# Optimization experiments

Measured on AMD Instinct MI355X. Metric: run time of the kernel, lower is better.

The kernel has to match this reference:

```python
import jax, jax.numpy as jnp
import numpy as np

N = 50000
E = 300000
HOPS = 3
LAYERS = 2
HEADS = 8
D_IN = 256
D_HID = 256
D_OUT = 256
D_HEAD = D_HID // HEADS
DECAY = [float(np.exp(-0.5 * k)) for k in range(HOPS)]  # hop_decay alpha = 0.5
LRELU_ACT = 0.01   # nn.LeakyReLU default slope (activation)
LRELU_ATT = 0.2    # GATConv attention leaky_relu slope
LN_EPS = 1e-5


def setup_inputs() -> dict:
    key = jax.random.key(0)
    ks = jax.random.split(key, 12)
    def sc(fan):
        return 1.0 / np.sqrt(fan)
    inp = {
        "x": jax.random.normal(ks[0], (N, D_IN), jnp.float32),
        "edge_index_k_hops": jax.random.randint(ks[1], (HOPS, 2, E), 0, N, jnp.int32),
        "lin1_w": jax.random.normal(ks[2], (D_IN, D_HID), jnp.float32) * sc(D_IN),
        "lin1_b": jnp.zeros((D_HID,), jnp.float32),
        "gat_w": jax.random.normal(ks[3], (LAYERS, HOPS, D_HID, D_HID), jnp.float32) * sc(D_HID),
        "gat_att_src": jax.random.normal(ks[4], (LAYERS, HOPS, HEADS, D_HEAD), jnp.float32) * sc(D_HEAD),
        "gat_att_dst": jax.random.normal(ks[5], (LAYERS, HOPS, HEADS, D_HEAD), jnp.float32) * sc(D_HEAD),
        "gat_bias": jnp.zeros((LAYERS, HOPS, D_HID), jnp.float32),
        "dec_w": jax.random.normal(ks[6], (LAYERS, HOPS, D_HID, D_OUT), jnp.float32) * sc(D_HID),
        "dec_b": jnp.zeros((LAYERS, HOPS, D_OUT), jnp.float32),
        "ln_scale": jnp.ones((LAYERS, D_OUT), jnp.float32),
        "ln_bias": jnp.zeros((LAYERS, D_OUT), jnp.float32),
    }
    return inp


def gat_conv(x, src, dst, W, a_src, a_dst, bias):
    # x: [N, D_HID]; src/dst: [E] ints. PyG GATConv (concat=True), eval mode.
    h = (x @ W).reshape(N, HEADS, D_HEAD)                  # [N, H, Dh]
    alpha_s = jnp.einsum('nhd,hd->nh', h, a_src)           # [N, H]
    alpha_d = jnp.einsum('nhd,hd->nh', h, a_dst)           # [N, H]
    e = jax.nn.leaky_relu(alpha_s[src] + alpha_d[dst], LRELU_ATT)  # [E, H]
    m = jax.ops.segment_max(e, dst, num_segments=N)        # segment softmax over dst
    e = jnp.exp(e - m[dst])
    s = jax.ops.segment_sum(e, dst, num_segments=N)
    a = e / (s[dst] + 1e-16)                               # [E, H]
    msg = h[src] * a[:, :, None]                           # [E, H, Dh]
    out = jax.ops.segment_sum(msg, dst, num_segments=N)    # [N, H, Dh]
    return out.reshape(N, D_HID) + bias


def layer_norm(x, scale, bias):
    mu = jnp.mean(x, axis=-1, keepdims=True)
    var = jnp.mean(jnp.square(x - mu), axis=-1, keepdims=True)
    return (x - mu) * jax.lax.rsqrt(var + LN_EPS) * scale + bias


def reference(x, edge_index_k_hops, lin1_w, lin1_b, gat_w, gat_att_src, gat_att_dst,
              gat_bias, dec_w, dec_b, ln_scale, ln_bias):
    h = jax.nn.leaky_relu(x @ lin1_w + lin1_b, LRELU_ACT)
    residual = h
    for l in range(LAYERS):
        acc = jnp.zeros((N, D_OUT), h.dtype)
        for k in range(HOPS):
            src = edge_index_k_hops[k, 0]
            dst = edge_index_k_hops[k, 1]
            xk = gat_conv(h, src, dst, gat_w[l, k], gat_att_src[l, k],
                          gat_att_dst[l, k], gat_bias[l, k])
            xk = jax.nn.leaky_relu(xk @ dec_w[l, k] + dec_b[l, k], LRELU_ACT)
            acc = acc + DECAY[k] * xk
        h = layer_norm(acc, ln_scale[l], ln_bias[l]) + residual
        residual = h
    return h
```

## Files before the change

kernel.cpp:

```cpp
#include <hip/hip_runtime.h>
#include <hip/hip_bf16.h>

#define NNODE 50000
#define NEDGE 300000
#define KPAD 40

static const float DECAY0 = 1.0f;
static const float DECAY1 = 0.60653065971263342f;
static const float DECAY2 = 0.36787944117144233f;

typedef __attribute__((ext_vector_type(8))) short bf16x8;
typedef __attribute__((ext_vector_type(4))) float f32x4;

__device__ __forceinline__ void split_bf16(float f, unsigned short& hi, unsigned short& lo) {
    const unsigned u = __float_as_uint(f);
    hi = (unsigned short)(u >> 16);
    const float fh = __uint_as_float((unsigned)hi << 16);
    lo = (unsigned short)(__float_as_uint(f - fh) >> 16);
}

__global__ __launch_bounds__(256) void transpose_w(
    const float* __restrict__ gat_w, const float* __restrict__ dec_w,
    const float* __restrict__ lin1_w, float* __restrict__ Wt)
{
    const int m = blockIdx.z;
    const float* src = (m < 6) ? gat_w + (size_t)m * 65536
                     : (m < 12) ? dec_w + (size_t)(m - 6) * 65536
                                : lin1_w;
    float* dst = Wt + (size_t)m * 65536;
    __shared__ float tile[32][33];
    const int bx = blockIdx.x * 32;
    const int by = blockIdx.y * 32;
    const int tx = threadIdx.x & 31;
    const int ty = threadIdx.x >> 5;
#pragma unroll
    for (int i = 0; i < 32; i += 8)
        tile[ty + i][tx] = src[(size_t)(by + ty + i) * 256 + bx + tx];
    __syncthreads();
#pragma unroll
    for (int i = 0; i < 32; i += 8)
        dst[(size_t)(bx + ty + i) * 256 + by + tx] = tile[tx][ty + i];
}

__global__ __launch_bounds__(256) void gemm_mfma(
    const float* __restrict__ A, const float* __restrict__ Wt, float* __restrict__ C,
    int M, const float* __restrict__ in_bias, const float* __restrict__ out_bias,
    float slope, int do_act, int accum, float decay)
{
    __shared__ unsigned short Ah[128][KPAD];
    __shared__ unsigned short Al[128][KPAD];
    __shared__ unsigned short Bh[128][KPAD];
    __shared__ unsigned short Bl[128][KPAD];

    const int tid  = threadIdx.x;
    const int bm   = blockIdx.x * 128;
    const int bn   = blockIdx.y * 128;
    const int lane = tid & 63;
    const int w    = tid >> 6;
    const int wm   = w >> 1, wn = w & 1;
    const int srow = tid >> 1;
    const int sks  = (tid & 1) << 4;

    f32x4 acc[4][4];
#pragma unroll
    for (int mi = 0; mi < 4; mi++)
#pragma unroll
        for (int ni = 0; ni < 4; ni++) {
            acc[mi][ni][0] = 0.f; acc[mi][ni][1] = 0.f;
            acc[mi][ni][2] = 0.f; acc[mi][ni][3] = 0.f;
        }

    const int lrow = lane & 15;
    const int koff = (lane >> 4) << 3;

    for (int k0 = 0; k0 < 256; k0 += 32) {
        __syncthreads();
        {
            float v[16];
            const int gr = bm + srow;
            if (gr < M) {
                const float* ap = A + (size_t)gr * 256 + k0 + sks;
                const float4 f0 = ((const float4*)ap)[0];
                const float4 f1 = ((const float4*)ap)[1];
                const float4 f2 = ((const float4*)ap)[2];
                const float4 f3 = ((const float4*)ap)[3];
                v[0]=f0.x; v[1]=f0.y; v[2]=f0.z; v[3]=f0.w;
                v[4]=f1.x; v[5]=f1.y; v[6]=f1.z; v[7]=f1.w;
                v[8]=f2.x; v[9]=f2.y; v[10]=f2.z; v[11]=f2.w;
                v[12]=f3.x; v[13]=f3.y; v[14]=f3.z; v[15]=f3.w;
            } else {
#pragma unroll
                for (int j = 0; j < 16; j++) v[j] = 0.f;
            }
            if (in_bias) {
#pragma unroll
                for (int j = 0; j < 16; j++) v[j] += in_bias[k0 + sks + j];
            }
            bf16x8 h0, h1, l0, l1;
#pragma unroll
            for (int j = 0; j < 8; j++) {
                unsigned short h, l;
                split_bf16(v[j], h, l);
                h0[j] = (short)h; l0[j] = (short)l;
            }
#pragma unroll
            for (int j = 0; j < 8; j++) {
                unsigned short h, l;
                split_bf16(v[8 + j], h, l);
                h1[j] = (short)h; l1[j] = (short)l;
            }
            *(bf16x8*)&Ah[srow][sks]     = h0;
            *(bf16x8*)&Ah[srow][sks + 8] = h1;
            *(bf16x8*)&Al[srow][sks]     = l0;
            *(bf16x8*)&Al[srow][sks + 8] = l1;
        }
        {
            const float* bp = Wt + (size_t)(bn + srow) * 256 + k0 + sks;
            const float4 f0 = ((const float4*)bp)[0];
            const float4 f1 = ((const float4*)bp)[1];
            const float4 f2 = ((const float4*)bp)[2];
            const float4 f3 = ((const float4*)bp)[3];
            float v[16];
            v[0]=f0.x; v[1]=f0.y; v[2]=f0.z; v[3]=f0.w;
            v[4]=f1.x; v[5]=f1.y; v[6]=f1.z; v[7]=f1.w;
            v[8]=f2.x; v[9]=f2.y; v[10]=f2.z; v[11]=f2.w;
            v[12]=f3.x; v[13]=f3.y; v[14]=f3.z; v[15]=f3.w;
            bf16x8 h0, h1, l0, l1;
#pragma unroll
            for (int j = 0; j < 8; j++) {
                unsigned short h, l;
                split_bf16(v[j], h, l);
                h0[j] = (short)h; l0[j] = (short)l;
            }
#pragma unroll
            for (int j = 0; j < 8; j++) {
                unsigned short h, l;
                split_bf16(v[8 + j], h, l);
                h1[j] = (short)h; l1[j] = (short)l;
            }
            *(bf16x8*)&Bh[srow][sks]     = h0;
            *(bf16x8*)&Bh[srow][sks + 8] = h1;
            *(bf16x8*)&Bl[srow][sks]     = l0;
            *(bf16x8*)&Bl[srow][sks + 8] = l1;
        }
        __syncthreads();
        bf16x8 ah[4], al[4];
#pragma unroll
        for (int mi = 0; mi < 4; mi++) {
            const int r = 64 * wm + 16 * mi + lrow;
            ah[mi] = *(const bf16x8*)&Ah[r][koff];
            al[mi] = *(const bf16x8*)&Al[r][koff];
        }
#pragma unroll
        for (int ni = 0; ni < 4; ni++) {
            const int r = 64 * wn + 16 * ni + lrow;
            const bf16x8 bh = *(const bf16x8*)&Bh[r][koff];
            const bf16x8 bl = *(const bf16x8*)&Bl[r][koff];
#pragma unroll
            for (int mi = 0; mi < 4; mi++) {
                acc[mi][ni] = __builtin_amdgcn_mfma_f32_16x16x32_bf16(ah[mi], bh, acc[mi][ni], 0, 0, 0);
                acc[mi][ni] = __builtin_amdgcn_mfma_f32_16x16x32_bf16(al[mi], bh, acc[mi][ni], 0, 0, 0);
                acc[mi][ni] = __builtin_amdgcn_mfma_f32_16x16x32_bf16(ah[mi], bl, acc[mi][ni], 0, 0, 0);
            }
        }
    }

    const int rb = bm + 64 * wm + ((lane >> 4) << 2);
    const int cb = bn + 64 * wn + (lane & 15);
#pragma unroll
    for (int ni = 0; ni < 4; ni++) {
        const int col = cb + 16 * ni;
        const float ob = out_bias ? out_bias[col] : 0.f;
#pragma unroll
        for (int mi = 0; mi < 4; mi++) {
#pragma unroll
            for (int r = 0; r < 4; r++) {
                const int row = rb + 16 * mi + r;
                if (row < M) {
                    float vv = acc[mi][ni][r] + ob;
                    if (do_act) vv = (vv > 0.f) ? vv : slope * vv;
                    vv *= decay;
                    float* cp = C + (size_t)row * 256 + col;
                    if (accum) *cp += vv; else *cp = vv;
                }
            }
        }
    }
}

__global__ __launch_bounds__(256) void alpha_kernel(
    const float* __restrict__ hproj, const float* __restrict__ att_s,
    const float* __restrict__ att_d, float* __restrict__ alpha_s, float* __restrict__ alpha_d)
{
    const int n = blockIdx.x;
    const int t = threadIdx.x;
    const float v  = hproj[(size_t)n * 256 + t];
    float ps = v * att_s[t];
    float pd = v * att_d[t];
#pragma unroll
    for (int off = 16; off > 0; off >>= 1) {
        ps += __shfl_xor(ps, off, 32);
        pd += __shfl_xor(pd, off, 32);
    }
    if ((t & 31) == 0) {
        alpha_s[n * 8 + (t >> 5)] = ps;
        alpha_d[n * 8 + (t >> 5)] = pd;
    }
}

__global__ __launch_bounds__(256) void hist_kernel(
    const int* __restrict__ edges, int* __restrict__ hist)
{
    const int gid = blockIdx.x * 256 + threadIdx.x;
    if (gid >= 3 * NEDGE) return;
    const int k = gid / NEDGE;
    const int e = gid - k * NEDGE;
    const int d = edges[(size_t)k * 2 * NEDGE + NEDGE + e];
    atomicAdd(&hist[k * NNODE + d], 1);
}

__global__ __launch_bounds__(1024) void scan_kernel(
    const int* __restrict__ hist, int* __restrict__ row_ptr)
{
    const int hop = blockIdx.x;
    const int* hsrc = hist + hop * NNODE;
    int* rp = row_ptr + hop * (NNODE + 1);
    __shared__ int buf[1024];
    const int t = threadIdx.x;
    int offset = 0;
    for (int base = 0; base < NNODE; base += 1024) {
        const int idx = base + t;
        int v = (idx < NNODE) ? hsrc[idx] : 0;
        buf[t] = v;
        __syncthreads();
        for (int off = 1; off < 1024; off <<= 1) {
            int add = (t >= off) ? buf[t - off] : 0;
            __syncthreads();
            buf[t] += add;
            __syncthreads();
        }
        if (idx < NNODE) rp[idx] = offset + buf[t] - v;
        const int total = buf[1023];
        __syncthreads();
        offset += total;
    }
    if (t == 0) rp[NNODE] = offset;
}

__global__ __launch_bounds__(256) void cursor_kernel(
    const int* __restrict__ row_ptr, int* __restrict__ cursor)
{
    const int gid = blockIdx.x * 256 + threadIdx.x;
    if (gid >= 3 * NNODE) return;
    const int k = gid / NNODE;
    const int i = gid - k * NNODE;
    cursor[gid] = row_ptr[k * (NNODE + 1) + i];
}

__global__ __launch_bounds__(256) void fill_kernel(
    const int* __restrict__ edges, int* __restrict__ cursor, int* __restrict__ col)
{
    const int gid = blockIdx.x * 256 + threadIdx.x;
    if (gid >= 3 * NEDGE) return;
    const int k = gid / NEDGE;
    const int e = gid - k * NEDGE;
    const int s = edges[(size_t)k * 2 * NEDGE + e];
    const int d = edges[(size_t)k * 2 * NEDGE + NEDGE + e];
    const int pos = atomicAdd(&cursor[k * NNODE + d], 1);
    col[(size_t)k * NEDGE + pos] = s;
}

__global__ __launch_bounds__(256) void gat_gather(
    const int* __restrict__ row_ptr, const int* __restrict__ col,
    const float* __restrict__ alpha_s, const float* __restrict__ alpha_d,
    const float* __restrict__ hproj, float* __restrict__ gat_out)
{
    const int wave = (blockIdx.x * 256 + threadIdx.x) >> 6;
    const int lane = threadIdx.x & 63;
    if (wave >= NNODE) return;
    const int d = wave;
    const int h = lane >> 3;
    const float adh = alpha_d[d * 8 + h];
    const int beg = row_ptr[d];
    const int end = row_ptr[d + 1];

    float m = -3.402823466e38f;
    float s = 0.f;
    float a0 = 0.f, a1 = 0.f, a2 = 0.f, a3 = 0.f;

    for (int e = beg; e < end; ++e) {
        const int sidx = col[e];
        float v = alpha_s[sidx * 8 + h] + adh;
        v = (v > 0.f) ? v : 0.2f * v;
        if (v > m) {
            const float f = __expf(m - v);
            s *= f; a0 *= f; a1 *= f; a2 *= f; a3 *= f;
            m = v;
        }
        const float p = __expf(v - m);
        s += p;
        const float4 hv = *reinterpret_cast<const float4*>(hproj + (size_t)sidx * 256 + lane * 4);
        a0 += p * hv.x; a1 += p * hv.y; a2 += p * hv.z; a3 += p * hv.w;
    }
    const float inv = 1.f / (s + 1e-16f);
    *reinterpret_cast<float4*>(gat_out + (size_t)d * 256 + lane * 4) =
        make_float4(a0 * inv, a1 * inv, a2 * inv, a3 * inv);
}

__global__ __launch_bounds__(256) void ln_kernel(
    const float* __restrict__ accb, float* __restrict__ h,
    const float* __restrict__ lns, const float* __restrict__ lnb)
{
    const int n = blockIdx.x;
    const int t = threadIdx.x;
    const float a = accb[(size_t)n * 256 + t];
    __shared__ float red[256];
    red[t] = a;
    __syncthreads();
    for (int off = 128; off > 0; off >>= 1) {
        if (t < off) red[t] += red[t + off];
        __syncthreads();
    }
    const float mu = red[0] * (1.f / 256.f);
    __syncthreads();
    const float dv = a - mu;
    red[t] = dv * dv;
    __syncthreads();
    for (int off = 128; off > 0; off >>= 1) {
        if (t < off) red[t] += red[t + off];
        __syncthreads();
    }
    const float var = red[0] * (1.f / 256.f);
    const float r = rsqrtf(var + 1e-5f);
    const size_t idx = (size_t)n * 256 + t;
    h[idx] = dv * r * lns[t] + lnb[t] + h[idx];
}

extern "C" void kernel_launch(void* const* d_in, const int* in_sizes, int n_in,
                              void* d_out, int out_size, void* d_ws, size_t ws_size,
                              hipStream_t stream) {
    const float* x      = (const float*)d_in[0];
    const int*   edges  = (const int*)  d_in[1];
    const float* lin1_w = (const float*)d_in[2];
    const float* lin1_b = (const float*)d_in[3];
    const float* gat_w  = (const float*)d_in[4];
    const float* att_s  = (const float*)d_in[5];
    const float* att_d  = (const float*)d_in[6];
    const float* gat_b  = (const float*)d_in[7];
    const float* dec_w  = (const float*)d_in[8];
    const float* dec_b  = (const float*)d_in[9];
    const float* ln_s   = (const float*)d_in[10];
    const float* ln_b   = (const float*)d_in[11];

    float* h = (float*)d_out;
    const size_t NF = (size_t)NNODE * 256;
    const size_t N8 = (size_t)NNODE * 8;

    float* acc_buf = (float*)d_ws;
    float* hproj   = acc_buf + NF;
    float* gat_out = hproj + NF;
    float* as_     = gat_out + NF;
    float* ad_     = as_ + N8;
    int*   hist    = (int*)(ad_ + N8);
    int*   cursor  = hist + 3 * NNODE;
    int*   row_ptr = cursor + 3 * NNODE;
    int*   col     = row_ptr + 3 * (NNODE + 1);
    float* Wt      = (float*)(col + 3 * NEDGE);

    const float decays[3] = {DECAY0, DECAY1, DECAY2};

    dim3 gg((NNODE + 127) / 128, 2);
    dim3 tg(8, 8, 13);
    const int e3b = (3 * NEDGE + 255) / 256;
    const int n3b = (3 * NNODE + 255) / 256;
    const int gb  = (NNODE * 64 + 255) / 256;

    transpose_w<<<tg, 256, 0, stream>>>(gat_w, dec_w, lin1_w, Wt);

    hipMemsetAsync(hist, 0, 3 * NNODE * sizeof(int), stream);
    hist_kernel<<<e3b, 256, 0, stream>>>(edges, hist);
    scan_kernel<<<3, 1024, 0, stream>>>(hist, row_ptr);
    cursor_kernel<<<n3b, 256, 0, stream>>>(row_ptr, cursor);
    fill_kernel<<<e3b, 256, 0, stream>>>(edges, cursor, col);

    gemm_mfma<<<gg, 256, 0, stream>>>(x, Wt + (size_t)12 * 65536, h, NNODE,
                                      nullptr, lin1_b, 0.01f, 1, 0, 1.f);

    for (int l = 0; l < 2; l++) {
        for (int k = 0; k < 3; k++) {
            const int lk = l * 3 + k;
            gemm_mfma<<<gg, 256, 0, stream>>>(h, Wt + (size_t)lk * 65536, hproj, NNODE,
                                              nullptr, nullptr, 0.f, 0, 0, 1.f);
            alpha_kernel<<<NNODE, 256, 0, stream>>>(hproj, att_s + lk * 256, att_d + lk * 256,
                                                    as_, ad_);
            gat_gather<<<gb, 256, 0, stream>>>(row_ptr + (size_t)k * (NNODE + 1),
                                               col + (size_t)k * NEDGE,
                                               as_, ad_, hproj, gat_out);
            gemm_mfma<<<gg, 256, 0, stream>>>(gat_out, Wt + (size_t)(6 + lk) * 65536, acc_buf,
                                              NNODE, gat_b + lk * 256, dec_b + lk * 256,
                                              0.01f, 1, (k > 0) ? 1 : 0, decays[k]);
        }
        ln_kernel<<<NNODE, 256, 0, stream>>>(acc_buf, h, ln_s + l * 256, ln_b + l * 256);
    }
}
```

Measured before the change: 1.723 ms.

## Store GEMM operands pre-split into packed bf16 hi/lo layout and prefetch tiles

Weights, the input x, the hidden state and the GAT output are now stored as packed bf16 hi/lo halves (512 shorts per row) by their producer kernels: the weight transpose, a new convert kernel, the gather epilogue, the GEMM epilogue and layernorm. The GEMM no longer does fp32 load plus split on every tile and instead loads bf16 directly, with a register prefetch of the next K-tile overlapping the MFMA work. The GAT bias is folded into the gather epilogue. This cuts redundant conversion work in every GEMM (each weight tile was re-split by every block), and the cost is a few extra conversion passes and scattered 2-byte epilogue stores.

Result: faster. 1.686 ms (-2.1%).

```diff
diff --git a/kernel.cpp b/kernel.cpp
--- a/kernel.cpp
+++ b/kernel.cpp
@@ -11,23 +11,28 @@
 
 typedef __attribute__((ext_vector_type(8))) short bf16x8;
 typedef __attribute__((ext_vector_type(4))) float f32x4;
-
-__device__ __forceinline__ void split_bf16(float f, unsigned short& hi, unsigned short& lo) {
+typedef __attribute__((ext_vector_type(4))) unsigned short u16x4;
+
+__device__ __forceinline__ unsigned split2(float f) {
     const unsigned u = __float_as_uint(f);
-    hi = (unsigned short)(u >> 16);
-    const float fh = __uint_as_float((unsigned)hi << 16);
-    lo = (unsigned short)(__float_as_uint(f - fh) >> 16);
-}
-
-__global__ __launch_bounds__(256) void transpose_w(
+    const unsigned hi = u >> 16;
+    const float fh = __uint_as_float(hi << 16);
+    const unsigned lo = __float_as_uint(f - fh) >> 16;
+    return (hi << 16) | lo;
+}
+__device__ __forceinline__ float bf2f(unsigned short u) {
+    return __uint_as_float((unsigned)u << 16);
+}
+
+__global__ __launch_bounds__(256) void transpose_split_w(
     const float* __restrict__ gat_w, const float* __restrict__ dec_w,
-    const float* __restrict__ lin1_w, float* __restrict__ Wt)
+    const float* __restrict__ lin1_w, unsigned short* __restrict__ Wp)
 {
     const int m = blockIdx.z;
     const float* src = (m < 6) ? gat_w + (size_t)m * 65536
                      : (m < 12) ? dec_w + (size_t)(m - 6) * 65536
                                 : lin1_w;
-    float* dst = Wt + (size_t)m * 65536;
+    unsigned short* dst = Wp + (size_t)m * 131072;
     __shared__ float tile[32][33];
     const int bx = blockIdx.x * 32;
     const int by = blockIdx.y * 32;
@@ -38,13 +43,42 @@
         tile[ty + i][tx] = src[(size_t)(by + ty + i) * 256 + bx + tx];
     __syncthreads();
 #pragma unroll
-    for (int i = 0; i < 32; i += 8)
-        dst[(size_t)(bx + ty + i) * 256 + by + tx] = tile[tx][ty + i];
-}
-
-__global__ __launch_bounds__(256) void gemm_mfma(
-    const float* __restrict__ A, const float* __restrict__ Wt, float* __restrict__ C,
-    int M, const float* __restrict__ in_bias, const float* __restrict__ out_bias,
+    for (int i = 0; i < 32; i += 8) {
+        const int n = bx + ty + i, k = by + tx;
+        const unsigned p = split2(tile[tx][ty + i]);
+        dst[(size_t)n * 512 + k] = (unsigned short)(p >> 16);
+        dst[(size_t)n * 512 + 256 + k] = (unsigned short)(p & 0xffffu);
+    }
+}
+
+__global__ __launch_bounds__(256) void convert_split(
+    const float* __restrict__ src, unsigned short* __restrict__ dst)
+{
+    const int gid = blockIdx.x * 256 + threadIdx.x;
+    if (gid >= NNODE * 32) return;
+    const int row = gid >> 5;
+    const int k = (gid & 31) * 8;
+    const float4 f0 = *reinterpret_cast<const float4*>(src + (size_t)row * 256 + k);
+    const float4 f1 = *reinterpret_cast<const float4*>(src + (size_t)row * 256 + k + 4);
+    u16x4 h0, h1, l0, l1;
+    unsigned p;
+    p = split2(f0.x); h0[0] = (unsigned short)(p >> 16); l0[0] = (unsigned short)p;
+    p = split2(f0.y); h0[1] = (unsigned short)(p >> 16); l0[1] = (unsigned short)p;
+    p = split2(f0.z); h0[2] = (unsigned short)(p >> 16); l0[2] = (unsigned short)p;
+    p = split2(f0.w); h0[3] = (unsigned short)(p >> 16); l0[3] = (unsigned short)p;
+    p = split2(f1.x); h1[0] = (unsigned short)(p >> 16); l1[0] = (unsigned short)p;
+    p = split2(f1.y); h1[1] = (unsigned short)(p >> 16); l1[1] = (unsigned short)p;
+    p = split2(f1.z); h1[2] = (unsigned short)(p >> 16); l1[2] = (unsigned short)p;
+    p = split2(f1.w); h1[3] = (unsigned short)(p >> 16); l1[3] = (unsigned short)p;
+    unsigned short* dh = dst + (size_t)row * 512 + k;
+    *(u16x4*)dh = h0; *(u16x4*)(dh + 4) = h1;
+    *(u16x4*)(dh + 256) = l0; *(u16x4*)(dh + 260) = l1;
+}
+
+__global__ __launch_bounds__(256) void gemm_pack(
+    const unsigned short* __restrict__ Ap, const unsigned short* __restrict__ Wp,
+    float* __restrict__ C, unsigned short* __restrict__ Cpack,
+    int M, const float* __restrict__ out_bias,
     float slope, int do_act, int accum, float decay)
 {
     __shared__ unsigned short Ah[128][KPAD];
@@ -59,7 +93,28 @@
     const int w    = tid >> 6;
     const int wm   = w >> 1, wn = w & 1;
     const int srow = tid >> 1;
-    const int sks  = (tid & 1) << 4;
+    const int skb  = (tid & 1) << 4;
+
+    const bool aval = (bm + srow) < M;
+    const unsigned short* ap = Ap + (size_t)(bm + srow) * 512 + skb;
+    const unsigned short* bp = Wp + (size_t)(bn + srow) * 512 + skb;
+
+    bf16x8 rAh0 = {0,0,0,0,0,0,0,0}, rAh1 = rAh0, rAl0 = rAh0, rAl1 = rAh0;
+    bf16x8 rBh0, rBh1, rBl0, rBl1;
+
+#define LOADT(K0)                                                        \
+    do {                                                                 \
+        if (aval) {                                                      \
+            rAh0 = *(const bf16x8*)(ap + (K0));                          \
+            rAh1 = *(const bf16x8*)(ap + (K0) + 8);                      \
+            rAl0 = *(const bf16x8*)(ap + 256 + (K0));                    \
+            rAl1 = *(const bf16x8*)(ap + 256 + (K0) + 8);                \
+        }                                                                \
+        rBh0 = *(const bf16x8*)(bp + (K0));                              \
+        rBh1 = *(const bf16x8*)(bp + (K0) + 8);                          \
+        rBl0 = *(const bf16x8*)(bp + 256 + (K0));                        \
+        rBl1 = *(const bf16x8*)(bp + 256 + (K0) + 8);                    \
+    } while (0)
 
     f32x4 acc[4][4];
 #pragma unroll
@@ -73,97 +128,42 @@
     const int lrow = lane & 15;
     const int koff = (lane >> 4) << 3;
 
-    for (int k0 = 0; k0 < 256; k0 += 32) {
-        __syncthreads();
-        {
-            float v[16];
-            const int gr = bm + srow;
-            if (gr < M) {
-                const float* ap = A + (size_t)gr * 256 + k0 + sks;
-                const float4 f0 = ((const float4*)ap)[0];
-                const float4 f1 = ((const float4*)ap)[1];
-                const float4 f2 = ((const float4*)ap)[2];
-                const float4 f3 = ((const float4*)ap)[3];
-                v[0]=f0.x; v[1]=f0.y; v[2]=f0.z; v[3]=f0.w;
-                v[4]=f1.x; v[5]=f1.y; v[6]=f1.z; v[7]=f1.w;
-                v[8]=f2.x; v[9]=f2.y; v[10]=f2.z; v[11]=f2.w;
-                v[12]=f3.x; v[13]=f3.y; v[14]=f3.z; v[15]=f3.w;
-            } else {
-#pragma unroll
-                for (int j = 0; j < 16; j++) v[j] = 0.f;
-            }
-            if (in_bias) {
-#pragma unroll
-                for (int j = 0; j < 16; j++) v[j] += in_bias[k0 + sks + j];
-            }
-            bf16x8 h0, h1, l0, l1;
-#pragma unroll
-            for (int j = 0; j < 8; j++) {
-                unsigned short h, l;
-                split_bf16(v[j], h, l);
-                h0[j] = (short)h; l0[j] = (short)l;
-            }
-#pragma unroll
-            for (int j = 0; j < 8; j++) {
-                unsigned short h, l;
-                split_bf16(v[8 + j], h, l);
-                h1[j] = (short)h; l1[j] = (short)l;
-            }
-            *(bf16x8*)&Ah[srow][sks]     = h0;
-            *(bf16x8*)&Ah[srow][sks + 8] = h1;
-            *(bf16x8*)&Al[srow][sks]     = l0;
-            *(bf16x8*)&Al[srow][sks + 8] = l1;
-        }
-        {
-            const float* bp = Wt + (size_t)(bn + srow) * 256 + k0 + sks;
-            const float4 f0 = ((const float4*)bp)[0];
-            const float4 f1 = ((const float4*)bp)[1];
-            const float4 f2 = ((const float4*)bp)[2];
-            const float4 f3 = ((const float4*)bp)[3];
-            float v[16];
-            v[0]=f0.x; v[1]=f0.y; v[2]=f0.z; v[3]=f0.w;
-            v[4]=f1.x; v[5]=f1.y; v[6]=f1.z; v[7]=f1.w;
-            v[8]=f2.x; v[9]=f2.y; v[10]=f2.z; v[11]=f2.w;
-            v[12]=f3.x; v[13]=f3.y; v[14]=f3.z; v[15]=f3.w;
-            bf16x8 h0, h1, l0, l1;
-#pragma unroll
-            for (int j = 0; j < 8; j++) {
-                unsigned short h, l;
-                split_bf16(v[j], h, l);
-                h0[j] = (short)h; l0[j] = (short)l;
-            }
-#pragma unroll
-            for (int j = 0; j < 8; j++) {
-                unsigned short h, l;
-                split_bf16(v[8 + j], h, l);
-                h1[j] = (short)h; l1[j] = (short)l;
-            }
-            *(bf16x8*)&Bh[srow][sks]     = h0;
-            *(bf16x8*)&Bh[srow][sks + 8] = h1;
-            *(bf16x8*)&Bl[srow][sks]     = l0;
-            *(bf16x8*)&Bl[srow][sks + 8] = l1;
-        }
-        __syncthreads();
-        bf16x8 ah[4], al[4];
+    LOADT(0);
+
+    for (int kt = 0; kt < 8; kt++) {
+        __syncthreads();
+        *(bf16x8*)&Ah[srow][skb]     = rAh0;
+        *(bf16x8*)&Ah[srow][skb + 8] = rAh1;
+        *(bf16x8*)&Al[srow][skb]     = rAl0;
+        *(bf16x8*)&Al[srow][skb + 8] = rAl1;
+        *(bf16x8*)&Bh[srow][skb]     = rBh0;
+        *(bf16x8*)&Bh[srow][skb + 8] = rBh1;
+        *(bf16x8*)&Bl[srow][skb]     = rBl0;
+        *(bf16x8*)&Bl[srow][skb + 8] = rBl1;
+        __syncthreads();
+        if (kt < 7) LOADT((kt + 1) * 32);
+
+        bf16x8 fah[4], fal[4];
 #pragma unroll
         for (int mi = 0; mi < 4; mi++) {
             const int r = 64 * wm + 16 * mi + lrow;
-            ah[mi] = *(const bf16x8*)&Ah[r][koff];
-            al[mi] = *(const bf16x8*)&Al[r][koff];
+            fah[mi] = *(const bf16x8*)&Ah[r][koff];
+            fal[mi] = *(const bf16x8*)&Al[r][koff];
         }
 #pragma unroll
         for (int ni = 0; ni < 4; ni++) {
             const int r = 64 * wn + 16 * ni + lrow;
-            const bf16x8 bh = *(const bf16x8*)&Bh[r][koff];
-            const bf16x8 bl = *(const bf16x8*)&Bl[r][koff];
+            const bf16x8 fbh = *(const bf16x8*)&Bh[r][koff];
+            const bf16x8 fbl = *(const bf16x8*)&Bl[r][koff];
 #pragma unroll
             for (int mi = 0; mi < 4; mi++) {
-                acc[mi][ni] = __builtin_amdgcn_mfma_f32_16x16x32_bf16(ah[mi], bh, acc[mi][ni], 0, 0, 0);
-                acc[mi][ni] = __builtin_amdgcn_mfma_f32_16x16x32_bf16(al[mi], bh, acc[mi][ni], 0, 0, 0);
-                acc[mi][ni] = __builtin_amdgcn_mfma_f32_16x16x32_bf16(ah[mi], bl, acc[mi][ni], 0, 0, 0);
+                acc[mi][ni] = __builtin_amdgcn_mfma_f32_16x16x32_bf16(fah[mi], fbh, acc[mi][ni], 0, 0, 0);
+                acc[mi][ni] = __builtin_amdgcn_mfma_f32_16x16x32_bf16(fal[mi], fbh, acc[mi][ni], 0, 0, 0);
+                acc[mi][ni] = __builtin_amdgcn_mfma_f32_16x16x32_bf16(fah[mi], fbl, acc[mi][ni], 0, 0, 0);
             }
         }
     }
+#undef LOADT
 
     const int rb = bm + 64 * wm + ((lane >> 4) << 2);
     const int cb = bn + 64 * wn + (lane & 15);
@@ -180,8 +180,15 @@
                     float vv = acc[mi][ni][r] + ob;
                     if (do_act) vv = (vv > 0.f) ? vv : slope * vv;
                     vv *= decay;
-                    float* cp = C + (size_t)row * 256 + col;
-                    if (accum) *cp += vv; else *cp = vv;
+                    if (Cpack) {
+                        const unsigned p = split2(vv);
+                        Cpack[(size_t)row * 512 + col] = (unsigned short)(p >> 16);
+                        Cpack[(size_t)row * 512 + 256 + col] = (unsigned short)(p & 0xffffu);
+                    } else if (accum) {
+                        C[(size_t)row * 256 + col] += vv;
+                    } else {
+                        C[(size_t)row * 256 + col] = vv;
+                    }
                 }
             }
         }
@@ -273,7 +280,8 @@
 __global__ __launch_bounds__(256) void gat_gather(
     const int* __restrict__ row_ptr, const int* __restrict__ col,
     const float* __restrict__ alpha_s, const float* __restrict__ alpha_d,
-    const float* __restrict__ hproj, float* __restrict__ gat_out)
+    const float* __restrict__ hproj, const float* __restrict__ bias,
+    unsigned short* __restrict__ outp)
 {
     const int wave = (blockIdx.x * 256 + threadIdx.x) >> 6;
     const int lane = threadIdx.x & 63;
@@ -303,12 +311,24 @@
         a0 += p * hv.x; a1 += p * hv.y; a2 += p * hv.z; a3 += p * hv.w;
     }
     const float inv = 1.f / (s + 1e-16f);
-    *reinterpret_cast<float4*>(gat_out + (size_t)d * 256 + lane * 4) =
-        make_float4(a0 * inv, a1 * inv, a2 * inv, a3 * inv);
+    const float b0 = bias[lane * 4 + 0], b1 = bias[lane * 4 + 1];
+    const float b2 = bias[lane * 4 + 2], b3 = bias[lane * 4 + 3];
+    u16x4 hi, lo;
+    unsigned p0 = split2(a0 * inv + b0);
+    unsigned p1 = split2(a1 * inv + b1);
+    unsigned p2 = split2(a2 * inv + b2);
+    unsigned p3 = split2(a3 * inv + b3);
+    hi[0] = (unsigned short)(p0 >> 16); lo[0] = (unsigned short)p0;
+    hi[1] = (unsigned short)(p1 >> 16); lo[1] = (unsigned short)p1;
+    hi[2] = (unsigned short)(p2 >> 16); lo[2] = (unsigned short)p2;
+    hi[3] = (unsigned short)(p3 >> 16); lo[3] = (unsigned short)p3;
+    *(u16x4*)(outp + (size_t)d * 512 + lane * 4) = hi;
+    *(u16x4*)(outp + (size_t)d * 512 + 256 + lane * 4) = lo;
 }
 
 __global__ __launch_bounds__(256) void ln_kernel(
-    const float* __restrict__ accb, float* __restrict__ h,
+    const float* __restrict__ accb, const unsigned short* __restrict__ hres,
+    unsigned short* __restrict__ hout, float* __restrict__ final_out,
     const float* __restrict__ lns, const float* __restrict__ lnb)
 {
     const int n = blockIdx.x;
@@ -332,8 +352,15 @@
     }
     const float var = red[0] * (1.f / 256.f);
     const float r = rsqrtf(var + 1e-5f);
-    const size_t idx = (size_t)n * 256 + t;
-    h[idx] = dv * r * lns[t] + lnb[t] + h[idx];
+    const float res = bf2f(hres[(size_t)n * 512 + t]) + bf2f(hres[(size_t)n * 512 + 256 + t]);
+    const float o = dv * r * lns[t] + lnb[t] + res;
+    if (final_out) {
+        final_out[(size_t)n * 256 + t] = o;
+    } else {
+        const unsigned p = split2(o);
+        hout[(size_t)n * 512 + t] = (unsigned short)(p >> 16);
+        hout[(size_t)n * 512 + 256 + t] = (unsigned short)(p & 0xffffu);
+    }
 }
 
 extern "C" void kernel_launch(void* const* d_in, const int* in_sizes, int n_in,
@@ -352,20 +379,22 @@
     const float* ln_s   = (const float*)d_in[10];
     const float* ln_b   = (const float*)d_in[11];
 
-    float* h = (float*)d_out;
+    float* out = (float*)d_out;
     const size_t NF = (size_t)NNODE * 256;
+    const size_t NP = (size_t)NNODE * 512;
     const size_t N8 = (size_t)NNODE * 8;
 
-    float* acc_buf = (float*)d_ws;
-    float* hproj   = acc_buf + NF;
-    float* gat_out = hproj + NF;
-    float* as_     = gat_out + NF;
-    float* ad_     = as_ + N8;
-    int*   hist    = (int*)(ad_ + N8);
-    int*   cursor  = hist + 3 * NNODE;
-    int*   row_ptr = cursor + 3 * NNODE;
-    int*   col     = row_ptr + 3 * (NNODE + 1);
-    float* Wt      = (float*)(col + 3 * NEDGE);
+    float*          acc_buf = (float*)d_ws;
+    float*          hproj   = acc_buf + NF;
+    unsigned short* gpack   = (unsigned short*)(hproj + NF);
+    unsigned short* hpack   = gpack + NP;
+    unsigned short* wpack   = hpack + NP;
+    float*          as_     = (float*)(wpack + (size_t)13 * 131072);
+    float*          ad_     = as_ + N8;
+    int*            hist    = (int*)(ad_ + N8);
+    int*            cursor  = hist + 3 * NNODE;
+    int*            row_ptr = cursor + 3 * NNODE;
+    int*            col     = row_ptr + 3 * (NNODE + 1);
 
     const float decays[3] = {DECAY0, DECAY1, DECAY2};
 
@@ -374,32 +403,36 @@
     const int e3b = (3 * NEDGE + 255) / 256;
     const int n3b = (3 * NNODE + 255) / 256;
     const int gb  = (NNODE * 64 + 255) / 256;
-
-    transpose_w<<<tg, 256, 0, stream>>>(gat_w, dec_w, lin1_w, Wt);
-
-    hipMemsetAsync(hist, 0, 3 * NNODE * sizeof(int), stream);
+    const int cvb = (NNODE * 32 + 255) / 256;
+
+    transpose_split_w<<<tg, 256, 0, stream>>>(gat_w, dec_w, lin1_w, wpack);
+    convert_split<<<cvb, 256, 0, stream>>>(x, gpack);
+
+    (void)hipMemsetAsync(hist, 0, 3 * NNODE * sizeof(int), stream);
     hist_kernel<<<e3b, 256, 0, stream>>>(edges, hist);
     scan_kernel<<<3, 1024, 0, stream>>>(hist, row_ptr);
     cursor_kernel<<<n3b, 256, 0, stream>>>(row_ptr, cursor);
     fill_kernel<<<e3b, 256, 0, stream>>>(edges, cursor, col);
 
-    gemm_mfma<<<gg, 256, 0, stream>>>(x, Wt + (size_t)12 * 65536, h, NNODE,
-                                      nullptr, lin1_b, 0.01f, 1, 0, 1.f);
+    gemm_pack<<<gg, 256, 0, stream>>>(gpack, wpack + (size_t)12 * 131072, nullptr, hpack,
+                                      NNODE, lin1_b, 0.01f, 1, 0, 1.f);
 
     for (int l = 0; l < 2; l++) {
         for (int k = 0; k < 3; k++) {
             const int lk = l * 3 + k;
-            gemm_mfma<<<gg, 256, 0, stream>>>(h, Wt + (size_t)lk * 65536, hproj, NNODE,
-                                              nullptr, nullptr, 0.f, 0, 0, 1.f);
+            gemm_pack<<<gg, 256, 0, stream>>>(hpack, wpack + (size_t)lk * 131072, hproj, nullptr,
+                                              NNODE, nullptr, 0.f, 0, 0, 1.f);
             alpha_kernel<<<NNODE, 256, 0, stream>>>(hproj, att_s + lk * 256, att_d + lk * 256,
                                                     as_, ad_);
             gat_gather<<<gb, 256, 0, stream>>>(row_ptr + (size_t)k * (NNODE + 1),
                                                col + (size_t)k * NEDGE,
-                                               as_, ad_, hproj, gat_out);
-            gemm_mfma<<<gg, 256, 0, stream>>>(gat_out, Wt + (size_t)(6 + lk) * 65536, acc_buf,
-                                              NNODE, gat_b + lk * 256, dec_b + lk * 256,
+                                               as_, ad_, hproj, gat_b + lk * 256, gpack);
+            gemm_pack<<<gg, 256, 0, stream>>>(gpack, wpack + (size_t)(6 + lk) * 131072, acc_buf,
+                                              nullptr, NNODE, dec_b + lk * 256,
                                               0.01f, 1, (k > 0) ? 1 : 0, decays[k]);
         }
-        ln_kernel<<<NNODE, 256, 0, stream>>>(acc_buf, h, ln_s + l * 256, ln_b + l * 256);
-    }
-}
+        ln_kernel<<<NNODE, 256, 0, stream>>>(acc_buf, hpack, hpack,
+                                             (l == 1) ? out : nullptr,
+                                             ln_s + l * 256, ln_b + l * 256);
+    }
+}
```
